# Kernel optimization log

Measured on AMD Instinct MI355X. Metric: run time of the kernel, lower is better.

## Reference

```python
import jax, jax.numpy as jnp
import numpy as np

B, C, NBLK = 512, 128, 6
VQC, EMB, K = 64, 128, 512
HW = 6
INPUT_SIZE = VQC * HW * HW  # 2304
COMMIT = 1.0
EPS = 1e-5


def conv3x3(x, w):
    # x: [N,C,H,W], w: [O,I,3,3], stride 1, pad 1, no bias
    return jax.lax.conv_general_dilated(x, w, (1, 1), 'SAME',
                                        dimension_numbers=('NCHW', 'OIHW', 'NCHW'))


def bn2d(x, scale, bias):
    # training-mode batch norm over (N,H,W), biased variance (matches torch)
    m = x.mean(axis=(0, 2, 3), keepdims=True)
    v = x.var(axis=(0, 2, 3), keepdims=True)
    return (x - m) * jax.lax.rsqrt(v + EPS) * scale[None, :, None, None] + bias[None, :, None, None]


def setup_inputs() -> dict:
    key = jax.random.key(0)
    ks = jax.random.split(key, 10)
    n = lambda k, shape, s=0.05: jax.random.normal(k, shape, jnp.float32) * s
    return {
        's0': jax.random.normal(ks[0], (B, C, HW, HW), jnp.float32),
        's1': jax.random.normal(ks[1], (B, C, HW, HW), jnp.float32),
        'conv_w': n(ks[2], (C, C, 3, 3)),
        'convs_w': n(ks[3], (C, C, 3, 3)),
        'rb_c1_w': n(ks[4], (NBLK, C, C, 3, 3)),
        'rb_bn1_s': jnp.ones((NBLK, C), jnp.float32),
        'rb_bn1_b': jnp.zeros((NBLK, C), jnp.float32),
        'rb_c2_w': n(ks[5], (NBLK, C, C, 3, 3)),
        'rb_bn2_s': jnp.ones((NBLK, C), jnp.float32),
        'rb_bn2_b': jnp.zeros((NBLK, C), jnp.float32),
        'conv_out_w': n(ks[6], (VQC, C, 3, 3)),
        'fc_w': n(ks[7], (EMB, INPUT_SIZE), 0.02),
        'fc_b': jnp.zeros((EMB,), jnp.float32),
        'emb': jax.random.uniform(ks[8], (K, EMB), jnp.float32, -1.0 / K, 1.0 / K),
    }


def reference(s0, s1, conv_w, convs_w, rb_c1_w, rb_bn1_s, rb_bn1_b,
              rb_c2_w, rb_bn2_s, rb_bn2_b, conv_out_w, fc_w, fc_b, emb):
    # stem: conv(s0) + conv_s(s1), relu
    x = jax.nn.relu(conv3x3(s0, conv_w) + conv3x3(s1, convs_w))
    # residual tower (fixed small loop over layers)
    for i in range(NBLK):
        idn = x
        h = jax.nn.relu(bn2d(conv3x3(x, rb_c1_w[i]), rb_bn1_s[i], rb_bn1_b[i]))
        h = bn2d(conv3x3(h, rb_c2_w[i]), rb_bn2_s[i], rb_bn2_b[i])
        x = jax.nn.relu(h + idn)
    x = conv3x3(x, conv_out_w)                         # [B, VQC, 6, 6]
    flat = x.reshape(-1, INPUT_SIZE) @ fc_w.T + fc_b   # [B, EMB]
    # bn_o: BatchNorm1d(affine=False), training mode
    fm = flat.mean(axis=0)
    fv = flat.var(axis=0)
    flat = (flat - fm) * jax.lax.rsqrt(fv + EPS)
    # VectorQuantizer1D
    d = (jnp.sum(flat ** 2, axis=1, keepdims=True)
         + jnp.sum(emb ** 2, axis=1)
         - 2.0 * flat @ emb.T)                         # [B, K]
    idx = jnp.argmin(d, axis=1)                        # [B]
    enc = jax.nn.one_hot(idx, K, dtype=flat.dtype)     # [B, K]
    q = enc @ emb                                      # [B, EMB]
    e_loss = jnp.mean((jax.lax.stop_gradient(q) - flat) ** 2, axis=1)
    q_loss = jnp.mean((q - jax.lax.stop_gradient(flat)) ** 2, axis=1)
    loss = q_loss + COMMIT * e_loss                    # [B]
    q_st = flat + jax.lax.stop_gradient(q - flat)      # straight-through
    avg_probs = enc.mean(axis=0)
    perplexity = jnp.exp(-jnp.sum(avg_probs * jnp.log(avg_probs + 1e-10)))
    z = jnp.broadcast_to(q_st[:, :, None, None], (q_st.shape[0], EMB, HW, HW))
    return z, loss, perplexity, idx
```

## Files before the change

kernel.cpp:

```cpp
#include <hip/hip_runtime.h>
#include <cstdint>
#include <cstddef>


typedef __attribute__((ext_vector_type(8))) short bf16x8;
typedef __attribute__((ext_vector_type(4))) float f32x4;

#define EPS_  1e-5f
#define NTOT_ 18432.0f

#define BUFA_OFF  3207168u
#define BUFB_OFF  5566464u
#define BUFC_OFF  7925760u
#define FLAT_OFF  BUFB_OFF
#define FCO_OFF   10285056u
#define STATS_OFF 10350592u

#define LOSS_OFF 2359296u
#define PERP_OFF 2359808u
#define IDX_OFF  2359809u

__device__ __forceinline__ unsigned short f2bf(float v) {
  unsigned u = __float_as_uint(v);
  return (unsigned short)((u + 0x7fffu + ((u >> 16) & 1u)) >> 16);
}
__device__ __forceinline__ float bf2f(unsigned short h) {
  return __uint_as_float((unsigned)h << 16);
}
__device__ __forceinline__ int swz16(int pr, int cio) {
  return (pr * 16 + cio) ^ ((pr ^ (pr >> 3)) & 7);
}

#define MF(Aa, Bb, Cc) Cc = __builtin_amdgcn_mfma_f32_16x16x32_bf16(Aa, Bb, Cc, 0, 0, 0)

__global__ __launch_bounds__(256) void prep_wb(
    const float* __restrict__ conv_w, const float* __restrict__ convs_w,
    const float* __restrict__ c1w, const float* __restrict__ c2w,
    const float* __restrict__ cow, uint4* __restrict__ wb) {
  const int ct = blockIdx.x * 4 + (threadIdx.x >> 6);
  const int lane = threadIdx.x & 63;
  const float* src;
  int n, ks_eff, chbase;
  if (ct < 576) {
    int ks = ct % 72;
    src = (ks < 36) ? conv_w : convs_w;
    ks_eff = (ks < 36) ? ks : ks - 36;
    n = (ct / 72) * 16 + (lane & 15);
    chbase = ct * 3;
  } else if (ct < 4032) {
    int q = ct - 576;
    int L = q / 288, r = q % 288;
    src = (L < 6) ? (c1w + (size_t)L * 147456u) : (c2w + (size_t)(L - 6) * 147456u);
    ks_eff = r % 36;
    n = (r / 36) * 16 + (lane & 15);
    chbase = 1728 + q * 3;
  } else {
    int q = ct - 4032;
    src = cow;
    ks_eff = q % 36;
    n = (q / 36) * 16 + (lane & 15);
    chbase = 12096 + q * 3;
  }
  const int tap = ks_eff >> 2;
  const int ci0 = (ks_eff & 3) * 32 + (lane >> 4) * 8;
  uint4 q1, q2, q3;
  unsigned* u1 = (unsigned*)&q1;
  unsigned* u2 = (unsigned*)&q2;
  unsigned* u3 = (unsigned*)&q3;
#pragma unroll
  for (int j = 0; j < 4; ++j) {
    float va = src[((size_t)n * 128 + ci0 + 2 * j) * 9 + tap];
    float vb = src[((size_t)n * 128 + ci0 + 2 * j + 1) * 9 + tap];
    unsigned short a1 = f2bf(va), b1 = f2bf(vb);
    float ra = va - bf2f(a1), rb = vb - bf2f(b1);
    unsigned short a2 = f2bf(ra), b2 = f2bf(rb);
    ra -= bf2f(a2); rb -= bf2f(b2);
    u1[j] = (unsigned)a1 | ((unsigned)b1 << 16);
    u2[j] = (unsigned)a2 | ((unsigned)b2 << 16);
    u3[j] = (unsigned)f2bf(ra) | ((unsigned)f2bf(rb) << 16);
  }
  wb[(size_t)(chbase + 0) * 64 + lane] = q1;
  wb[(size_t)(chbase + 1) * 64 + lane] = q2;
  wb[(size_t)(chbase + 2) * 64 + lane] = q3;
}

template <int MODE, int NTILES, int STATS, int OUTFLAT>
__global__ __launch_bounds__(256) void conv_mfma(
    const float* __restrict__ in, const float* __restrict__ idn,
    float* __restrict__ xback, const uint4* __restrict__ wbL,
    const float* __restrict__ stats_in, const float* __restrict__ gamma,
    const float* __restrict__ beta, float* __restrict__ out,
    float* __restrict__ stats_out) {
  constexpr int NTPW = NTILES / 4;
  __shared__ __align__(16) unsigned short apl[3 * 8192];
  __shared__ __align__(16) float As[128], Bs[128];
  const int t = threadIdx.x, b = blockIdx.x;

  if (MODE >= 1 && t < 128) {
    float m = stats_in[t] * (1.0f / NTOT_);
    float var = stats_in[128 + t] * (1.0f / NTOT_) - m * m;
    float A = rsqrtf(var + EPS_) * gamma[t];
    As[t] = A;
    Bs[t] = fmaf(-m, A, beta[t]);
  }
  uint4* z4 = (uint4*)apl;
  for (int i = t; i < 3072; i += 256) z4[i] = make_uint4(0, 0, 0, 0);
  __syncthreads();

  const float4* in4 = (const float4*)in;
  const float4* idn4 = (const float4*)idn;
  float4* xb4 = (float4*)xback;
  const float4* As4 = (const float4*)As;
  const float4* Bs4 = (const float4*)Bs;
  for (int e = t; e < 576; e += 256) {
    int px = e >> 4, cich = e & 15;
    size_t gi = (size_t)(b * 36 + px) * 32 + cich * 2;
    float4 v0 = in4[gi], v1 = in4[gi + 1];
    if (MODE >= 1) {
      float4 A0 = As4[cich * 2], B0 = Bs4[cich * 2];
      float4 A1 = As4[cich * 2 + 1], B1 = Bs4[cich * 2 + 1];
      v0.x = fmaf(v0.x, A0.x, B0.x); v0.y = fmaf(v0.y, A0.y, B0.y);
      v0.z = fmaf(v0.z, A0.z, B0.z); v0.w = fmaf(v0.w, A0.w, B0.w);
      v1.x = fmaf(v1.x, A1.x, B1.x); v1.y = fmaf(v1.y, A1.y, B1.y);
      v1.z = fmaf(v1.z, A1.z, B1.z); v1.w = fmaf(v1.w, A1.w, B1.w);
      if (MODE == 2) {
        float4 d0 = idn4[gi], d1 = idn4[gi + 1];
        v0.x += d0.x; v0.y += d0.y; v0.z += d0.z; v0.w += d0.w;
        v1.x += d1.x; v1.y += d1.y; v1.z += d1.z; v1.w += d1.w;
      }
      v0.x = fmaxf(v0.x, 0.f); v0.y = fmaxf(v0.y, 0.f);
      v0.z = fmaxf(v0.z, 0.f); v0.w = fmaxf(v0.w, 0.f);
      v1.x = fmaxf(v1.x, 0.f); v1.y = fmaxf(v1.y, 0.f);
      v1.z = fmaxf(v1.z, 0.f); v1.w = fmaxf(v1.w, 0.f);
      if (MODE == 2) { xb4[gi] = v0; xb4[gi + 1] = v1; }
    }
    float vv[8] = {v0.x, v0.y, v0.z, v0.w, v1.x, v1.y, v1.z, v1.w};
    uint4 q1, q2, q3;
    unsigned* u1 = (unsigned*)&q1;
    unsigned* u2 = (unsigned*)&q2;
    unsigned* u3 = (unsigned*)&q3;
#pragma unroll
    for (int j = 0; j < 4; ++j) {
      unsigned short a1 = f2bf(vv[2 * j]), b1 = f2bf(vv[2 * j + 1]);
      float ra = vv[2 * j] - bf2f(a1), rb = vv[2 * j + 1] - bf2f(b1);
      unsigned short a2 = f2bf(ra), b2 = f2bf(rb);
      ra -= bf2f(a2); rb -= bf2f(b2);
      u1[j] = (unsigned)a1 | ((unsigned)b1 << 16);
      u2[j] = (unsigned)a2 | ((unsigned)b2 << 16);
      u3[j] = (unsigned)f2bf(ra) | ((unsigned)f2bf(rb) << 16);
    }
    int hh = px / 6, ww = px - hh * 6;
    int pp = (hh + 1) * 8 + (ww + 1);
    int a16 = swz16(pp, cich);
    z4[0 * 1024 + a16] = q1;
    z4[1 * 1024 + a16] = q2;
    z4[2 * 1024 + a16] = q3;
  }
  __syncthreads();

  const int wave = t >> 6, lane = t & 63;
  const int l15 = lane & 15, kq = lane >> 4;
  int ppb[3];
#pragma unroll
  for (int mt = 0; mt < 3; ++mt) {
    int px = mt * 16 + l15;
    ppb[mt] = (px < 36) ? ((px / 6 + 1) * 8 + (px % 6) + 1) : 9;
  }
  f32x4 zz = {0.f, 0.f, 0.f, 0.f};
  f32x4 acc[3][NTPW];
#pragma unroll
  for (int mt = 0; mt < 3; ++mt)
#pragma unroll
    for (int n2 = 0; n2 < NTPW; ++n2) acc[mt][n2] = zz;

  for (int tap = 0; tap < 9; ++tap) {
    const int dyx = (tap / 3 - 1) * 8 + (tap % 3) - 1;
#pragma unroll
    for (int kc = 0; kc < 4; ++kc) {
      const int ks = tap * 4 + kc;
      bf16x8 bfr[NTPW][3];
#pragma unroll
      for (int n2 = 0; n2 < NTPW; ++n2)
#pragma unroll
        for (int pl = 0; pl < 3; ++pl)
          bfr[n2][pl] = __builtin_bit_cast(bf16x8,
              wbL[((size_t)((wave * NTPW + n2) * 36 + ks) * 3 + pl) * 64 + lane]);
      bf16x8 afr[3][3];
#pragma unroll
      for (int mt = 0; mt < 3; ++mt) {
        int pr = ppb[mt] + dyx;
        int a16 = swz16(pr, kc * 4 + kq);
#pragma unroll
        for (int pl = 0; pl < 3; ++pl)
          afr[mt][pl] = *(const bf16x8*)(apl + pl * 8192 + a16 * 8);
      }
#pragma unroll
      for (int mt = 0; mt < 3; ++mt)
#pragma unroll
        for (int n2 = 0; n2 < NTPW; ++n2) {
          MF(afr[mt][0], bfr[n2][0], acc[mt][n2]);
          MF(afr[mt][1], bfr[n2][0], acc[mt][n2]);
          MF(afr[mt][0], bfr[n2][1], acc[mt][n2]);
          MF(afr[mt][2], bfr[n2][0], acc[mt][n2]);
          MF(afr[mt][1], bfr[n2][1], acc[mt][n2]);
          MF(afr[mt][0], bfr[n2][2], acc[mt][n2]);
        }
    }
  }

  float s[NTPW], sq[NTPW];
#pragma unroll
  for (int n2 = 0; n2 < NTPW; ++n2) { s[n2] = 0.f; sq[n2] = 0.f; }
#pragma unroll
  for (int mt = 0; mt < 3; ++mt)
#pragma unroll
    for (int n2 = 0; n2 < NTPW; ++n2) {
      const int cc = (wave * NTPW + n2) * 16 + l15;
#pragma unroll
      for (int q = 0; q < 4; ++q) {
        int px = mt * 16 + kq * 4 + q;
        float v = acc[mt][n2][q];
        if (px < 36) {
          if (OUTFLAT) out[(size_t)b * 2304 + cc * 36 + px] = v;
          else out[((size_t)b * 36 + px) * 128 + cc] = v;
          s[n2] += v; sq[n2] = fmaf(v, v, sq[n2]);
        }
      }
    }
  if (STATS) {
#pragma unroll
    for (int n2 = 0; n2 < NTPW; ++n2) {
      float sv = s[n2], qv = sq[n2];
      sv += __shfl_xor(sv, 16); qv += __shfl_xor(qv, 16);
      sv += __shfl_xor(sv, 32); qv += __shfl_xor(qv, 32);
      if (kq == 0) {
        const int cc = (wave * NTPW + n2) * 16 + l15;
        atomicAdd(&stats_out[cc], sv);
        atomicAdd(&stats_out[128 + cc], qv);
      }
    }
  }
}

__global__ __launch_bounds__(256) void stem_mfma(
    const float* __restrict__ s0, const float* __restrict__ s1,
    const uint4* __restrict__ wbL, float* __restrict__ out) {
  __shared__ __align__(16) unsigned short apl[3 * 8192];
  const int t = threadIdx.x, b = blockIdx.x;
  uint4* z4 = (uint4*)apl;
  for (int i = t; i < 3072; i += 256) z4[i] = make_uint4(0, 0, 0, 0);

  const int wave = t >> 6, lane = t & 63;
  const int l15 = lane & 15, kq = lane >> 4;
  int ppb[3];
#pragma unroll
  for (int mt = 0; mt < 3; ++mt) {
    int px = mt * 16 + l15;
    ppb[mt] = (px < 36) ? ((px / 6 + 1) * 8 + (px % 6) + 1) : 9;
  }
  f32x4 zz = {0.f, 0.f, 0.f, 0.f};
  f32x4 acc[3][2];
#pragma unroll
  for (int mt = 0; mt < 3; ++mt) { acc[mt][0] = zz; acc[mt][1] = zz; }

  for (int pass = 0; pass < 2; ++pass) {
    __syncthreads();
    const float* sp = pass ? s1 : s0;
    for (int e = t; e < 4608; e += 256) {
      int c = e / 36, px = e - c * 36;
      int hh = px / 6, ww = px - hh * 6;
      int pp = (hh + 1) * 8 + (ww + 1);
      int sw = swz16(pp, c >> 3) * 8 + (c & 7);
      float v0 = sp[(size_t)b * 4608 + e];
      unsigned short h; float r;
      h = f2bf(v0); apl[0 * 8192 + sw] = h; r = v0 - bf2f(h);
      h = f2bf(r);  apl[1 * 8192 + sw] = h; r -= bf2f(h);
      apl[2 * 8192 + sw] = f2bf(r);
    }
    __syncthreads();

    for (int tap = 0; tap < 9; ++tap) {
      const int dyx = (tap / 3 - 1) * 8 + (tap % 3) - 1;
#pragma unroll
      for (int kc = 0; kc < 4; ++kc) {
        const int ks = pass * 36 + tap * 4 + kc;
        bf16x8 bfr[2][3];
#pragma unroll
        for (int n2 = 0; n2 < 2; ++n2)
#pragma unroll
          for (int pl = 0; pl < 3; ++pl)
            bfr[n2][pl] = __builtin_bit_cast(bf16x8,
                wbL[((size_t)((wave * 2 + n2) * 72 + ks) * 3 + pl) * 64 + lane]);
        bf16x8 afr[3][3];
#pragma unroll
        for (int mt = 0; mt < 3; ++mt) {
          int pr = ppb[mt] + dyx;
          int a16 = swz16(pr, kc * 4 + kq);
#pragma unroll
          for (int pl = 0; pl < 3; ++pl)
            afr[mt][pl] = *(const bf16x8*)(apl + pl * 8192 + a16 * 8);
        }
#pragma unroll
        for (int mt = 0; mt < 3; ++mt)
#pragma unroll
          for (int n2 = 0; n2 < 2; ++n2) {
            MF(afr[mt][0], bfr[n2][0], acc[mt][n2]);
            MF(afr[mt][1], bfr[n2][0], acc[mt][n2]);
            MF(afr[mt][0], bfr[n2][1], acc[mt][n2]);
            MF(afr[mt][2], bfr[n2][0], acc[mt][n2]);
            MF(afr[mt][1], bfr[n2][1], acc[mt][n2]);
            MF(afr[mt][0], bfr[n2][2], acc[mt][n2]);
          }
      }
    }
  }
#pragma unroll
  for (int mt = 0; mt < 3; ++mt)
#pragma unroll
    for (int n2 = 0; n2 < 2; ++n2) {
      const int cc = (wave * 2 + n2) * 16 + l15;
#pragma unroll
      for (int q = 0; q < 4; ++q) {
        int px = mt * 16 + kq * 4 + q;
        if (px < 36)
          out[((size_t)b * 36 + px) * 128 + cc] = fmaxf(acc[mt][n2][q], 0.f);
      }
    }
}

__global__ __launch_bounds__(256) void fc_kernel(
    const float* __restrict__ flat, const float* __restrict__ fcw,
    float* __restrict__ out) {
  __shared__ __align__(16) float fs[32 * 384];
  const int t = threadIdx.x;
  const int b0 = blockIdx.x * 32;
  const int k04 = blockIdx.y * 96;
  float4* fs4 = (float4*)fs;
  const float4* fl4 = (const float4*)flat;
  for (int i = t; i < 3072; i += 256) {
    int r = i / 96, k = i - r * 96;
    fs4[i] = fl4[(size_t)(b0 + r) * 576 + k04 + k];
  }
  __syncthreads();
  const int tc = t & 31, tp = t >> 5;
  const float4* fw4 = (const float4*)fcw;
  float acc[4][4];
#pragma unroll
  for (int r = 0; r < 4; ++r)
#pragma unroll
    for (int j = 0; j < 4; ++j) acc[r][j] = 0.f;
  for (int k = 0; k < 96; ++k) {
    float4 w[4];
#pragma unroll
    for (int j = 0; j < 4; ++j) w[j] = fw4[(size_t)(tc + 32 * j) * 576 + k04 + k];
    float4 x[4];
#pragma unroll
    for (int r = 0; r < 4; ++r) x[r] = fs4[(tp * 4 + r) * 96 + k];
#pragma unroll
    for (int r = 0; r < 4; ++r)
#pragma unroll
      for (int j = 0; j < 4; ++j) {
        acc[r][j] = fmaf(x[r].x, w[j].x, acc[r][j]);
        acc[r][j] = fmaf(x[r].y, w[j].y, acc[r][j]);
        acc[r][j] = fmaf(x[r].z, w[j].z, acc[r][j]);
        acc[r][j] = fmaf(x[r].w, w[j].w, acc[r][j]);
      }
  }
#pragma unroll
  for (int r = 0; r < 4; ++r)
#pragma unroll
    for (int j = 0; j < 4; ++j)
      atomicAdd(&out[(size_t)(b0 + tp * 4 + r) * 128 + tc + 32 * j], acc[r][j]);
}

__global__ __launch_bounds__(64) void fcstats_kernel(const float* __restrict__ fco,
                                                     float* __restrict__ st) {
  const int e = blockIdx.x, l = threadIdx.x;
  float s = 0.f, q = 0.f;
  for (int b = l; b < 512; b += 64) {
    float v = fco[(size_t)b * 128 + e];
    s += v; q = fmaf(v, v, q);
  }
  for (int off = 32; off; off >>= 1) {
    s += __shfl_down(s, off);
    q += __shfl_down(q, off);
  }
  if (l == 0) { st[e] = s; st[128 + e] = q; }
}

__global__ __launch_bounds__(256) void vq_kernel(
    const float* __restrict__ fco, const float* __restrict__ st,
    const float* __restrict__ emb, float* __restrict__ dout) {
  __shared__ __align__(16) float fn[128], qv[128];
  __shared__ unsigned long long wmin[4];
  __shared__ float lred[2];
  const int t = threadIdx.x, b = blockIdx.x;
  if (t < 128) {
    float m = st[t] * (1.0f / 512.0f);
    float var = st[128 + t] * (1.0f / 512.0f) - m * m;
    float rs = rsqrtf(var + EPS_);
    fn[t] = (fco[(size_t)b * 128 + t] - m) * rs;
  }
  __syncthreads();
  const float4* e4 = (const float4*)emb;
  const float4* f4 = (const float4*)fn;
  unsigned long long best = ~0ull;
  for (int k = t; k < 512; k += 256) {
    float d = 0.f;
#pragma unroll 4
    for (int j = 0; j < 32; ++j) {
      float4 e = e4[(size_t)k * 32 + j];
      float4 f = f4[j];
      float dx = f.x - e.x, dy = f.y - e.y, dz = f.z - e.z, dw = f.w - e.w;
      d = fmaf(dx, dx, d); d = fmaf(dy, dy, d);
      d = fmaf(dz, dz, d); d = fmaf(dw, dw, d);
    }
    unsigned long long key = ((unsigned long long)__float_as_uint(d) << 32) | (unsigned)k;
    if (key < best) best = key;
  }
  for (int off = 32; off; off >>= 1) {
    unsigned long long o = __shfl_down(best, off);
    if (o < best) best = o;
  }
  if ((t & 63) == 0) wmin[t >> 6] = best;
  __syncthreads();
  if (t == 0) {
    unsigned long long m01 = wmin[0] < wmin[1] ? wmin[0] : wmin[1];
    unsigned long long m23 = wmin[2] < wmin[3] ? wmin[2] : wmin[3];
    wmin[0] = m01 < m23 ? m01 : m23;
  }
  __syncthreads();
  const int ks = (int)(wmin[0] & 0xffffffffu);
  if (t < 128) qv[t] = emb[(size_t)ks * 128 + t];
  __syncthreads();
  if (t < 128) {
    float df = qv[t] - fn[t];
    float sq = df * df;
    for (int off = 32; off; off >>= 1) sq += __shfl_down(sq, off);
    if ((t & 63) == 0) lred[t >> 6] = sq;
  }
  __syncthreads();
  if (t == 0) dout[LOSS_OFF + b] = (lred[0] + lred[1]) * (2.0f / 128.0f);
  float4* z4 = (float4*)dout;
  for (int i = t; i < 1152; i += 256) {
    int e = i / 9, j = i - e * 9;
    float v = qv[e];
    z4[((size_t)b * 128 + e) * 9 + j] = make_float4(v, v, v, v);
  }
  if (t == 0) dout[IDX_OFF + b] = (float)ks;
}

__global__ __launch_bounds__(512) void perp_kernel(float* __restrict__ dout) {
  __shared__ int hist[512];
  __shared__ float wr[8];
  const int t = threadIdx.x;
  hist[t] = 0;
  __syncthreads();
  int k = (int)dout[IDX_OFF + t];
  atomicAdd(&hist[k], 1);
  __syncthreads();
  float p = hist[t] * (1.0f / 512.0f);
  float term = p * logf(p + 1e-10f);
  for (int off = 32; off; off >>= 1) term += __shfl_down(term, off);
  if ((t & 63) == 0) wr[t >> 6] = term;
  __syncthreads();
  if (t == 0) {
    float s = 0.f;
#pragma unroll
    for (int i = 0; i < 8; ++i) s += wr[i];
    dout[PERP_OFF] = expf(-s);
  }
}

extern "C" void kernel_launch(void* const* d_in, const int* in_sizes, int n_in,
                              void* d_out, int out_size, void* d_ws, size_t ws_size,
                              hipStream_t stream) {
  const float* s0        = (const float*)d_in[0];
  const float* s1        = (const float*)d_in[1];
  const float* conv_w    = (const float*)d_in[2];
  const float* convs_w   = (const float*)d_in[3];
  const float* rb_c1_w   = (const float*)d_in[4];
  const float* rb_bn1_s  = (const float*)d_in[5];
  const float* rb_bn1_b  = (const float*)d_in[6];
  const float* rb_c2_w   = (const float*)d_in[7];
  const float* rb_bn2_s  = (const float*)d_in[8];
  const float* rb_bn2_b  = (const float*)d_in[9];
  const float* conv_out_w= (const float*)d_in[10];
  const float* fc_w      = (const float*)d_in[11];
  const float* emb       = (const float*)d_in[13];

  float* ws   = (float*)d_ws;
  uint4* wb   = (uint4*)d_ws;
  float* bufA = ws + BUFA_OFF;
  float* bufB = ws + BUFB_OFF;
  float* bufC = ws + BUFC_OFF;
  float* flat = ws + FLAT_OFF;
  float* fco  = ws + FCO_OFF;
  float* stats= ws + STATS_OFF;
  float* out  = (float*)d_out;

  hipMemsetAsync(fco, 0, (65536 + 3328) * sizeof(float), stream);

  prep_wb<<<1044, 256, 0, stream>>>(conv_w, convs_w, rb_c1_w, rb_c2_w,
                                    conv_out_w, wb);
  stem_mfma<<<512, 256, 0, stream>>>(s0, s1, wb, bufA);

  for (int i = 0; i < 6; ++i) {
    float* st1 = stats + (size_t)(2 * i) * 256;
    float* st2 = stats + (size_t)(2 * i + 1) * 256;
    const uint4* wb1 = wb + (size_t)(1728 + i * 864) * 64;
    const uint4* wb2 = wb + (size_t)(1728 + (6 + i) * 864) * 64;
    if (i == 0) {
      conv_mfma<0, 8, 1, 0><<<512, 256, 0, stream>>>(
          bufA, nullptr, nullptr, wb1, nullptr, nullptr, nullptr, bufB, st1);
    } else {
      conv_mfma<2, 8, 1, 0><<<512, 256, 0, stream>>>(
          bufC, bufA, bufA, wb1, stats + (size_t)(2 * i - 1) * 256,
          rb_bn2_s + (size_t)(i - 1) * 128, rb_bn2_b + (size_t)(i - 1) * 128,
          bufB, st1);
    }
    conv_mfma<1, 8, 1, 0><<<512, 256, 0, stream>>>(
        bufB, nullptr, nullptr, wb2, st1,
        rb_bn1_s + (size_t)i * 128, rb_bn1_b + (size_t)i * 128, bufC, st2);
  }

  conv_mfma<2, 4, 0, 1><<<512, 256, 0, stream>>>(
      bufC, bufA, bufA, wb + (size_t)12096 * 64, stats + 11u * 256,
      rb_bn2_s + 5u * 128, rb_bn2_b + 5u * 128, flat, nullptr);

  fc_kernel<<<dim3(16, 6), 256, 0, stream>>>(flat, fc_w, fco);
  fcstats_kernel<<<128, 64, 0, stream>>>(fco, stats + 12u * 256);
  vq_kernel<<<512, 256, 0, stream>>>(fco, stats + 12u * 256, emb, out);
  perp_kernel<<<1, 512, 0, stream>>>(out);
}
```

Baseline: 782.7 us.

## Split conv output channels across a second grid dimension with ping-pong identity buffers

```diff
diff --git a/kernel.cpp b/kernel.cpp
--- a/kernel.cpp
+++ b/kernel.cpp
@@ -15,6 +15,8 @@
 #define FLAT_OFF  BUFB_OFF
 #define FCO_OFF   10285056u
 #define STATS_OFF 10350592u
+#define BUFD_OFF  10353920u
+#define WS_NEED_SPLIT  (12713216ull * 4ull)
 
 #define LOSS_OFF 2359296u
 #define PERP_OFF 2359808u
@@ -28,7 +30,7 @@
   return __uint_as_float((unsigned)h << 16);
 }
 __device__ __forceinline__ int swz16(int pr, int cio) {
-  return (pr * 16 + cio) ^ ((pr ^ (pr >> 3)) & 7);
+  return pr * 16 + (cio ^ ((pr + 6 * (pr >> 3)) & 7));
 }
 
 #define MF(Aa, Bb, Cc) Cc = __builtin_amdgcn_mfma_f32_16x16x32_bf16(Aa, Bb, Cc, 0, 0, 0)
@@ -94,7 +96,8 @@
   constexpr int NTPW = NTILES / 4;
   __shared__ __align__(16) unsigned short apl[3 * 8192];
   __shared__ __align__(16) float As[128], Bs[128];
-  const int t = threadIdx.x, b = blockIdx.x;
+  const int t = threadIdx.x, b = blockIdx.x, nb = blockIdx.y;
+  const uint4* wbB = wbL + (size_t)nb * (NTILES * 36 * 3) * 64;
 
   if (MODE >= 1 && t < 128) {
     float m = stats_in[t] * (1.0f / NTOT_);
@@ -131,8 +134,8 @@
       v0.x = fmaxf(v0.x, 0.f); v0.y = fmaxf(v0.y, 0.f);
       v0.z = fmaxf(v0.z, 0.f); v0.w = fmaxf(v0.w, 0.f);
       v1.x = fmaxf(v1.x, 0.f); v1.y = fmaxf(v1.y, 0.f);
-      v1.z = fmaxf(v1.z, 0.f); v1.w = fmaxf(v1.w, 0.f);
-      if (MODE == 2) { xb4[gi] = v0; xb4[gi + 1] = v1; }
+      v1.w = fmaxf(v1.w, 0.f); v1.z = fmaxf(v1.z, 0.f);
+      if (MODE == 2 && nb == 0) { xb4[gi] = v0; xb4[gi + 1] = v1; }
     }
     float vv[8] = {v0.x, v0.y, v0.z, v0.w, v1.x, v1.y, v1.z, v1.w};
     uint4 q1, q2, q3;
@@ -184,7 +187,7 @@
 #pragma unroll
         for (int pl = 0; pl < 3; ++pl)
           bfr[n2][pl] = __builtin_bit_cast(bf16x8,
-              wbL[((size_t)((wave * NTPW + n2) * 36 + ks) * 3 + pl) * 64 + lane]);
+              wbB[((size_t)((wave * NTPW + n2) * 36 + ks) * 3 + pl) * 64 + lane]);
       bf16x8 afr[3][3];
 #pragma unroll
       for (int mt = 0; mt < 3; ++mt) {
@@ -215,7 +218,7 @@
   for (int mt = 0; mt < 3; ++mt)
 #pragma unroll
     for (int n2 = 0; n2 < NTPW; ++n2) {
-      const int cc = (wave * NTPW + n2) * 16 + l15;
+      const int cc = nb * (NTILES * 16) + (wave * NTPW + n2) * 16 + l15;
 #pragma unroll
       for (int q = 0; q < 4; ++q) {
         int px = mt * 16 + kq * 4 + q;
@@ -234,7 +237,7 @@
       sv += __shfl_xor(sv, 16); qv += __shfl_xor(qv, 16);
       sv += __shfl_xor(sv, 32); qv += __shfl_xor(qv, 32);
       if (kq == 0) {
-        const int cc = (wave * NTPW + n2) * 16 + l15;
+        const int cc = nb * (NTILES * 16) + (wave * NTPW + n2) * 16 + l15;
         atomicAdd(&stats_out[cc], sv);
         atomicAdd(&stats_out[128 + cc], qv);
       }
@@ -246,7 +249,8 @@
     const float* __restrict__ s0, const float* __restrict__ s1,
     const uint4* __restrict__ wbL, float* __restrict__ out) {
   __shared__ __align__(16) unsigned short apl[3 * 8192];
-  const int t = threadIdx.x, b = blockIdx.x;
+  const int t = threadIdx.x, b = blockIdx.x, nb = blockIdx.y;
+  const uint4* wbB = wbL + (size_t)nb * (4 * 72 * 3) * 64;
   uint4* z4 = (uint4*)apl;
   for (int i = t; i < 3072; i += 256) z4[i] = make_uint4(0, 0, 0, 0);
 
@@ -259,9 +263,9 @@
     ppb[mt] = (px < 36) ? ((px / 6 + 1) * 8 + (px % 6) + 1) : 9;
   }
   f32x4 zz = {0.f, 0.f, 0.f, 0.f};
-  f32x4 acc[3][2];
-#pragma unroll
-  for (int mt = 0; mt < 3; ++mt) { acc[mt][0] = zz; acc[mt][1] = zz; }
+  f32x4 acc[3];
+#pragma unroll
+  for (int mt = 0; mt < 3; ++mt) acc[mt] = zz;
 
   for (int pass = 0; pass < 2; ++pass) {
     __syncthreads();
@@ -284,13 +288,11 @@
 #pragma unroll
       for (int kc = 0; kc < 4; ++kc) {
         const int ks = pass * 36 + tap * 4 + kc;
-        bf16x8 bfr[2][3];
-#pragma unroll
-        for (int n2 = 0; n2 < 2; ++n2)
-#pragma unroll
-          for (int pl = 0; pl < 3; ++pl)
-            bfr[n2][pl] = __builtin_bit_cast(bf16x8,
-                wbL[((size_t)((wave * 2 + n2) * 72 + ks) * 3 + pl) * 64 + lane]);
+        bf16x8 bfr[3];
+#pragma unroll
+        for (int pl = 0; pl < 3; ++pl)
+          bfr[pl] = __builtin_bit_cast(bf16x8,
+              wbB[((size_t)(wave * 72 + ks) * 3 + pl) * 64 + lane]);
         bf16x8 afr[3][3];
 #pragma unroll
         for (int mt = 0; mt < 3; ++mt) {
@@ -301,31 +303,27 @@
             afr[mt][pl] = *(const bf16x8*)(apl + pl * 8192 + a16 * 8);
         }
 #pragma unroll
-        for (int mt = 0; mt < 3; ++mt)
-#pragma unroll
-          for (int n2 = 0; n2 < 2; ++n2) {
-            MF(afr[mt][0], bfr[n2][0], acc[mt][n2]);
-            MF(afr[mt][1], bfr[n2][0], acc[mt][n2]);
-            MF(afr[mt][0], bfr[n2][1], acc[mt][n2]);
-            MF(afr[mt][2], bfr[n2][0], acc[mt][n2]);
-            MF(afr[mt][1], bfr[n2][1], acc[mt][n2]);
-            MF(afr[mt][0], bfr[n2][2], acc[mt][n2]);
-          }
+        for (int mt = 0; mt < 3; ++mt) {
+          MF(afr[mt][0], bfr[0], acc[mt]);
+          MF(afr[mt][1], bfr[0], acc[mt]);
+          MF(afr[mt][0], bfr[1], acc[mt]);
+          MF(afr[mt][2], bfr[0], acc[mt]);
+          MF(afr[mt][1], bfr[1], acc[mt]);
+          MF(afr[mt][0], bfr[2], acc[mt]);
+        }
       }
     }
   }
 #pragma unroll
-  for (int mt = 0; mt < 3; ++mt)
-#pragma unroll
-    for (int n2 = 0; n2 < 2; ++n2) {
-      const int cc = (wave * 2 + n2) * 16 + l15;
-#pragma unroll
-      for (int q = 0; q < 4; ++q) {
-        int px = mt * 16 + kq * 4 + q;
-        if (px < 36)
-          out[((size_t)b * 36 + px) * 128 + cc] = fmaxf(acc[mt][n2][q], 0.f);
-      }
-    }
+  for (int mt = 0; mt < 3; ++mt) {
+    const int cc = nb * 64 + wave * 16 + l15;
+#pragma unroll
+    for (int q = 0; q < 4; ++q) {
+      int px = mt * 16 + kq * 4 + q;
+      if (px < 36)
+        out[((size_t)b * 36 + px) * 128 + cc] = fmaxf(acc[mt][q], 0.f);
+    }
+  }
 }
 
 __global__ __launch_bounds__(256) void fc_kernel(
@@ -494,16 +492,19 @@
   float* bufA = ws + BUFA_OFF;
   float* bufB = ws + BUFB_OFF;
   float* bufC = ws + BUFC_OFF;
+  float* bufD = ws + BUFD_OFF;
   float* flat = ws + FLAT_OFF;
   float* fco  = ws + FCO_OFF;
   float* stats= ws + STATS_OFF;
   float* out  = (float*)d_out;
 
+  const bool split2 = (ws_size >= (size_t)WS_NEED_SPLIT);
+
   hipMemsetAsync(fco, 0, (65536 + 3328) * sizeof(float), stream);
 
   prep_wb<<<1044, 256, 0, stream>>>(conv_w, convs_w, rb_c1_w, rb_c2_w,
                                     conv_out_w, wb);
-  stem_mfma<<<512, 256, 0, stream>>>(s0, s1, wb, bufA);
+  stem_mfma<<<dim3(512, 2), 256, 0, stream>>>(s0, s1, wb, bufA);
 
   for (int i = 0; i < 6; ++i) {
     float* st1 = stats + (size_t)(2 * i) * 256;
@@ -511,21 +512,29 @@
     const uint4* wb1 = wb + (size_t)(1728 + i * 864) * 64;
     const uint4* wb2 = wb + (size_t)(1728 + (6 + i) * 864) * 64;
     if (i == 0) {
-      conv_mfma<0, 8, 1, 0><<<512, 256, 0, stream>>>(
+      conv_mfma<0, 4, 1, 0><<<dim3(512, 2), 256, 0, stream>>>(
           bufA, nullptr, nullptr, wb1, nullptr, nullptr, nullptr, bufB, st1);
+    } else if (split2) {
+      float* idn_i = (i & 1) ? bufA : bufD;
+      float* xbk_i = (i & 1) ? bufD : bufA;
+      conv_mfma<2, 4, 1, 0><<<dim3(512, 2), 256, 0, stream>>>(
+          bufC, idn_i, xbk_i, wb1, stats + (size_t)(2 * i - 1) * 256,
+          rb_bn2_s + (size_t)(i - 1) * 128, rb_bn2_b + (size_t)(i - 1) * 128,
+          bufB, st1);
     } else {
-      conv_mfma<2, 8, 1, 0><<<512, 256, 0, stream>>>(
+      conv_mfma<2, 8, 1, 0><<<dim3(512, 1), 256, 0, stream>>>(
           bufC, bufA, bufA, wb1, stats + (size_t)(2 * i - 1) * 256,
           rb_bn2_s + (size_t)(i - 1) * 128, rb_bn2_b + (size_t)(i - 1) * 128,
           bufB, st1);
     }
-    conv_mfma<1, 8, 1, 0><<<512, 256, 0, stream>>>(
+    conv_mfma<1, 4, 1, 0><<<dim3(512, 2), 256, 0, stream>>>(
         bufB, nullptr, nullptr, wb2, st1,
         rb_bn1_s + (size_t)i * 128, rb_bn1_b + (size_t)i * 128, bufC, st2);
   }
 
-  conv_mfma<2, 4, 0, 1><<<512, 256, 0, stream>>>(
-      bufC, bufA, bufA, wb + (size_t)12096 * 64, stats + 11u * 256,
+  float* x5 = split2 ? bufD : bufA;
+  conv_mfma<2, 4, 0, 1><<<dim3(512, 1), 256, 0, stream>>>(
+      bufC, x5, bufA, wb + (size_t)12096 * 64, stats + 11u * 256,
       rb_bn2_s + 5u * 128, rb_bn2_b + 5u * 128, flat, nullptr);
 
   fc_kernel<<<dim3(16, 6), 256, 0, stream>>>(flat, fc_w, fco);
```

After: 844.1 us. 7.8% more time.
